# Optimization experiments

Hardware: AMD Instinct MI355X
Metric: run time of the kernel (lower is better)

The kernel has to match this reference:

```python
import jax, jax.numpy as jnp
import numpy as np

H_DIM, N_HEAD, FF_DIM, B_GRAPHS, MAX_N = 256, 8, 1024, 16, 512
LENGTHS = np.array([512, 480, 448, 416, 384, 352, 320, 288] * 2)  # ragged graph sizes, sum = 6400
N_NODES = int(LENGTHS.sum())
N_EDGES = 16 * N_NODES  # avg degree 16


def setup_inputs() -> dict:
    key = jax.random.key(0)
    kq, kk, kv, ko, k1, k2, kh = jax.random.split(key, 7)
    offsets = np.concatenate([[0], np.cumsum(LENGTHS)[:-1]])
    batch_np = np.repeat(np.arange(B_GRAPHS), LENGTHS)
    rng = np.random.default_rng(0)
    src = rng.integers(0, N_NODES, N_EDGES)
    g = batch_np[src]
    dst = offsets[g] + rng.integers(0, LENGTHS[g])  # dst in same graph as src
    edge_index = jnp.asarray(np.stack([src, dst]), dtype=jnp.int32)
    batch = jnp.asarray(batch_np, dtype=jnp.int32)

    def w(k, shape):
        return 0.02 * jax.random.normal(k, shape, dtype=jnp.float32)

    return dict(
        h=jax.random.normal(kh, (N_NODES, H_DIM), dtype=jnp.float32),
        Wq=w(kq, (H_DIM, H_DIM)), bq=jnp.zeros(H_DIM),
        Wk=w(kk, (H_DIM, H_DIM)), bk=jnp.zeros(H_DIM),
        Wv=w(kv, (H_DIM, H_DIM)), bv=jnp.zeros(H_DIM),
        Wo=w(ko, (H_DIM, H_DIM)), bo=jnp.zeros(H_DIM),
        W1=w(k1, (FF_DIM, H_DIM)), b1=jnp.zeros(FF_DIM),
        W2=w(k2, (H_DIM, FF_DIM)), b2=jnp.zeros(H_DIM),
        g1=jnp.ones(H_DIM), be1=jnp.zeros(H_DIM),
        g2=jnp.ones(H_DIM), be2=jnp.zeros(H_DIM),
        batch=batch, edge_index=edge_index,
        num_graphs=B_GRAPHS, max_n=MAX_N, n_head=N_HEAD,
    )


def _layernorm(x, g, b, eps=1e-5):
    mu = x.mean(-1, keepdims=True)
    var = ((x - mu) ** 2).mean(-1, keepdims=True)
    return (x - mu) * jax.lax.rsqrt(var + eps) * g + b


def reference(h, Wq, bq, Wk, bk, Wv, bv, Wo, bo, W1, b1, W2, b2, g1, be1, g2, be2,
              batch, edge_index, num_graphs, max_n, n_head):
    N, H = h.shape
    dh = H // n_head
    # position of each node inside its graph (batch is sorted by graph)
    counts = jax.ops.segment_sum(jnp.ones(N, jnp.int32), batch, num_segments=num_graphs)
    offsets = jnp.concatenate([jnp.zeros(1, jnp.int32), jnp.cumsum(counts)[:-1].astype(jnp.int32)])
    pos = jnp.arange(N, dtype=jnp.int32) - offsets[batch]
    # to_dense_batch: pad ragged nodes into [B, S, H]
    x = jnp.zeros((num_graphs, max_n, H), h.dtype).at[batch, pos].set(h)
    # to_dense_adj + _canonical_mask: faithful to source, EDGES get -inf (True -> -inf)
    src, dst = edge_index[0], edge_index[1]
    adj = jnp.zeros((num_graphs, max_n, max_n), bool).at[batch[src], pos[src], pos[dst]].set(True)
    attn_mask = jnp.where(adj, -jnp.inf, 0.0)[:, None, :, :]  # [B,1,S,S], broadcast over heads

    def proj(W, b):
        return (x @ W.T + b).reshape(num_graphs, max_n, n_head, dh).transpose(0, 2, 1, 3)

    q = proj(Wq, bq)
    k = proj(Wk, bk)
    v = proj(Wk, bk)  # faithful to source: V_x uses self.K
    scores = jax.nn.softmax(attn_mask + jnp.einsum('bhsd,bhtd->bhst', q, k) / np.sqrt(dh).astype(h.dtype), axis=-1)
    att = jnp.einsum('bhst,bhtd->bhsd', scores, v).transpose(0, 2, 1, 3).reshape(num_graphs, max_n, H)
    att = att @ Wo.T + bo
    h_att = att[batch, pos]  # from_dense_batch: unpad back to [N, H]
    h1 = _layernorm(h_att + h, g1, be1)
    ff = jax.nn.relu(h1 @ W1.T + b1) @ W2.T + b2
    return _layernorm(ff + h1, g2, be2)
```

## Files before the change

### kernel.cpp

```cpp
#include <hip/hip_runtime.h>
#include <math.h>

typedef unsigned int u32;
typedef unsigned short ushort_t;
typedef __attribute__((ext_vector_type(8))) short short8;
typedef __attribute__((ext_vector_type(4))) float f32x4;
typedef __attribute__((ext_vector_type(16))) float f32x16;

#define B_G 16
#define S_MAX 512
#define NH 8
#define DH 32
#define HD 256
#define FFD 1024
#define ADJW 16

__device__ __forceinline__ ushort_t f2bf(float f) {
  u32 u = __float_as_uint(f);
  u += 0x7fffu + ((u >> 16) & 1u);
  return (ushort_t)(u >> 16);
}
__device__ __forceinline__ float bf2f(ushort_t s) {
  return __uint_as_float(((u32)s) << 16);
}

__device__ __forceinline__ void gll16(const void* g, void* l) {
  __builtin_amdgcn_global_load_lds(
      (const __attribute__((address_space(1))) unsigned int*)g,
      (__attribute__((address_space(3))) unsigned int*)l, 16, 0, 0);
}

__global__ __launch_bounds__(256) void k_prep2(u32* __restrict__ adj,
    const int* __restrict__ batch, int N, int* __restrict__ offs,
    const float* __restrict__ bq, const float* __restrict__ bk, float* __restrict__ bqk,
    const float* __restrict__ wa, const float* __restrict__ wb, const float* __restrict__ wc,
    const float* __restrict__ wd, const float* __restrict__ we,
    ushort_t* __restrict__ oa, ushort_t* __restrict__ ob, ushort_t* __restrict__ oc,
    ushort_t* __restrict__ od, ushort_t* __restrict__ oe,
    const float* __restrict__ h, ushort_t* __restrict__ hb) {
  int blk = blockIdx.x, tid = threadIdx.x;
  if (blk < 128) {
    uint4 z = {0u, 0u, 0u, 0u};
    ((uint4*)adj)[blk * 256 + tid] = z;
  } else if (blk == 128) {
    bqk[tid] = bq[tid];
    bqk[HD + tid] = bk[tid];
    if (tid <= B_G) {
      if (tid == B_G) { offs[B_G] = N; }
      else {
        int lo = 0, hi = N;
        while (lo < hi) { int mid = (lo + hi) >> 1; if (batch[mid] < tid) lo = mid + 1; else hi = mid; }
        offs[tid] = lo;
      }
    }
  } else if (blk < 481) {
    int bb = blk - 129;
    const float* src; ushort_t* dst; int off;
    if (bb < 32)       { src = wa; dst = oa; off = bb; }
    else if (bb < 64)  { src = wb; dst = ob; off = bb - 32; }
    else if (bb < 96)  { src = wc; dst = oc; off = bb - 64; }
    else if (bb < 224) { src = wd; dst = od; off = bb - 96; }
    else               { src = we; dst = oe; off = bb - 224; }
    size_t i = (size_t)off * 2048 + tid * 8;
    float4 v0 = *(const float4*)&src[i];
    float4 v1 = *(const float4*)&src[i + 4];
    uint4 pk;
    pk.x = (u32)f2bf(v0.x) | ((u32)f2bf(v0.y) << 16);
    pk.y = (u32)f2bf(v0.z) | ((u32)f2bf(v0.w) << 16);
    pk.z = (u32)f2bf(v1.x) | ((u32)f2bf(v1.y) << 16);
    pk.w = (u32)f2bf(v1.z) | ((u32)f2bf(v1.w) << 16);
    *(uint4*)&dst[i] = pk;
  } else {
    size_t i = ((size_t)(blk - 481) * 256 + tid) * 8;
    float4 v0 = *(const float4*)&h[i];
    float4 v1 = *(const float4*)&h[i + 4];
    uint4 pk;
    pk.x = (u32)f2bf(v0.x) | ((u32)f2bf(v0.y) << 16);
    pk.y = (u32)f2bf(v0.z) | ((u32)f2bf(v0.w) << 16);
    pk.z = (u32)f2bf(v1.x) | ((u32)f2bf(v1.y) << 16);
    pk.w = (u32)f2bf(v1.z) | ((u32)f2bf(v1.w) << 16);
    *(uint4*)&hb[i] = pk;
  }
}

__global__ __launch_bounds__(256) void k_qk(const ushort_t* __restrict__ A,
    const ushort_t* __restrict__ W, const float* __restrict__ bias,
    ushort_t* __restrict__ Cout, int gridx,
    const int* __restrict__ ei, int E, const int* __restrict__ batch,
    const int* __restrict__ offs, u32* __restrict__ adj) {
  __shared__ __align__(16) ushort_t As[2][64 * 64];
  __shared__ __align__(16) ushort_t Bs[2][128 * 64];
  int tid = threadIdx.x;
  int wid = tid >> 6, lane = tid & 63;
  int wm = wid & 1, wn = wid >> 1;
  int arow0 = blockIdx.x * 64, bcol0 = blockIdx.y * 128;

  {
    int e = (blockIdx.y * gridx + blockIdx.x) * 256 + tid;
    if (e < E) {
      int s = ei[e], d = ei[E + e];
      int b = batch[s];
      int o = offs[b];
      atomicOr(&adj[(b * S_MAX + (s - o)) * ADJW + ((d - o) >> 5)], 1u << ((d - o) & 31));
    }
  }

  const ushort_t* gA[2]; const ushort_t* gB[4];
  int dofsA[2], dofsB[4];
  #pragma unroll
  for (int i = 0; i < 2; i++) {
    int s = i * 256 + wid * 64 + lane;
    int r = s >> 3, ck = (s & 7) ^ (r & 7);
    gA[i] = A + (size_t)(arow0 + r) * HD + ck * 8;
    dofsA[i] = (i * 256 + wid * 64) * 8;
  }
  #pragma unroll
  for (int i = 0; i < 4; i++) {
    int s = i * 256 + wid * 64 + lane;
    int r = s >> 3, ck = (s & 7) ^ (r & 7);
    gB[i] = W + (size_t)(bcol0 + r) * HD + ck * 8;
    dofsB[i] = (i * 256 + wid * 64) * 8;
  }

  f32x4 acc[2][4];
  #pragma unroll
  for (int i = 0; i < 2; i++)
    #pragma unroll
    for (int j = 0; j < 4; j++) { f32x4 z = {0.f,0.f,0.f,0.f}; acc[i][j] = z; }

  #pragma unroll
  for (int i = 0; i < 2; i++) gll16(gA[i], &As[0][dofsA[i]]);
  #pragma unroll
  for (int i = 0; i < 4; i++) gll16(gB[i], &Bs[0][dofsB[i]]);
  asm volatile("s_waitcnt vmcnt(0)" ::: "memory");
  __builtin_amdgcn_s_barrier();

  int cur = 0;
  for (int ks = 0; ks < 4; ks++) {
    if (ks < 3) {
      int k0n = (ks + 1) << 6;
      #pragma unroll
      for (int i = 0; i < 2; i++) gll16(gA[i] + k0n, &As[cur ^ 1][dofsA[i]]);
      #pragma unroll
      for (int i = 0; i < 4; i++) gll16(gB[i] + k0n, &Bs[cur ^ 1][dofsB[i]]);
      asm volatile("s_waitcnt vmcnt(6)" ::: "memory");
    } else {
      asm volatile("s_waitcnt vmcnt(0)" ::: "memory");
    }
    __builtin_amdgcn_s_barrier();
    #pragma unroll
    for (int kk = 0; kk < 2; kk++) {
      short8 af[2], bfv[4];
      #pragma unroll
      for (int i = 0; i < 2; i++) {
        int row = wm * 32 + i * 16 + (lane & 15);
        int ck = (kk * 4 + (lane >> 4)) ^ (row & 7);
        af[i] = *(const short8*)&As[cur][row * 64 + ck * 8];
      }
      #pragma unroll
      for (int j = 0; j < 4; j++) {
        int row = wn * 64 + j * 16 + (lane & 15);
        int ck = (kk * 4 + (lane >> 4)) ^ (row & 7);
        bfv[j] = *(const short8*)&Bs[cur][row * 64 + ck * 8];
      }
      #pragma unroll
      for (int i = 0; i < 2; i++)
        #pragma unroll
        for (int j = 0; j < 4; j++)
          acc[i][j] = __builtin_amdgcn_mfma_f32_16x16x32_bf16(af[i], bfv[j], acc[i][j], 0, 0, 0);
    }
    __builtin_amdgcn_s_barrier();
    cur ^= 1;
  }

  float bj[4]; int colb[4];
  #pragma unroll
  for (int j = 0; j < 4; j++) {
    colb[j] = bcol0 + wn * 64 + j * 16 + (lane & 15);
    bj[j] = bias[colb[j]];
  }
  #pragma unroll
  for (int i = 0; i < 2; i++) {
    #pragma unroll
    for (int r = 0; r < 4; r++) {
      int row = arow0 + wm * 32 + i * 16 + (lane >> 4) * 4 + r;
      #pragma unroll
      for (int j = 0; j < 4; j++)
        Cout[(size_t)row * 512 + colb[j]] = f2bf(acc[i][j][r] + bj[j]);
    }
  }
}

__global__ __launch_bounds__(256) void k_ffup(const ushort_t* __restrict__ A,
    const ushort_t* __restrict__ W, const float* __restrict__ bias,
    ushort_t* __restrict__ Cout, int Ncols, int Kdim) {
  __shared__ __align__(16) ushort_t As[2][64 * 64];
  __shared__ __align__(16) ushort_t Bs[2][128 * 64];
  int tid = threadIdx.x;
  int wid = tid >> 6, lane = tid & 63;
  int wm = wid & 1, wn = wid >> 1;
  int arow0 = blockIdx.x * 64, bcol0 = blockIdx.y * 128;

  const ushort_t* gA[2]; const ushort_t* gB[4];
  int dofsA[2], dofsB[4];
  #pragma unroll
  for (int i = 0; i < 2; i++) {
    int s = i * 256 + wid * 64 + lane;
    int r = s >> 3, ck = (s & 7) ^ (r & 7);
    gA[i] = A + (size_t)(arow0 + r) * Kdim + ck * 8;
    dofsA[i] = (i * 256 + wid * 64) * 8;
  }
  #pragma unroll
  for (int i = 0; i < 4; i++) {
    int s = i * 256 + wid * 64 + lane;
    int r = s >> 3, ck = (s & 7) ^ (r & 7);
    gB[i] = W + (size_t)(bcol0 + r) * Kdim + ck * 8;
    dofsB[i] = (i * 256 + wid * 64) * 8;
  }

  f32x4 acc[2][4];
  #pragma unroll
  for (int i = 0; i < 2; i++)
    #pragma unroll
    for (int j = 0; j < 4; j++) { f32x4 z = {0.f,0.f,0.f,0.f}; acc[i][j] = z; }

  #pragma unroll
  for (int i = 0; i < 2; i++) gll16(gA[i], &As[0][dofsA[i]]);
  #pragma unroll
  for (int i = 0; i < 4; i++) gll16(gB[i], &Bs[0][dofsB[i]]);
  asm volatile("s_waitcnt vmcnt(0)" ::: "memory");
  __builtin_amdgcn_s_barrier();

  int nsteps = Kdim >> 6;
  int cur = 0;
  for (int ks = 0; ks < nsteps; ks++) {
    if (ks + 1 < nsteps) {
      int k0n = (ks + 1) << 6;
      #pragma unroll
      for (int i = 0; i < 2; i++) gll16(gA[i] + k0n, &As[cur ^ 1][dofsA[i]]);
      #pragma unroll
      for (int i = 0; i < 4; i++) gll16(gB[i] + k0n, &Bs[cur ^ 1][dofsB[i]]);
      asm volatile("s_waitcnt vmcnt(6)" ::: "memory");
    } else {
      asm volatile("s_waitcnt vmcnt(0)" ::: "memory");
    }
    __builtin_amdgcn_s_barrier();
    #pragma unroll
    for (int kk = 0; kk < 2; kk++) {
      short8 af[2], bfv[4];
      #pragma unroll
      for (int i = 0; i < 2; i++) {
        int row = wm * 32 + i * 16 + (lane & 15);
        int ck = (kk * 4 + (lane >> 4)) ^ (row & 7);
        af[i] = *(const short8*)&As[cur][row * 64 + ck * 8];
      }
      #pragma unroll
      for (int j = 0; j < 4; j++) {
        int row = wn * 64 + j * 16 + (lane & 15);
        int ck = (kk * 4 + (lane >> 4)) ^ (row & 7);
        bfv[j] = *(const short8*)&Bs[cur][row * 64 + ck * 8];
      }
      #pragma unroll
      for (int i = 0; i < 2; i++)
        #pragma unroll
        for (int j = 0; j < 4; j++)
          acc[i][j] = __builtin_amdgcn_mfma_f32_16x16x32_bf16(af[i], bfv[j], acc[i][j], 0, 0, 0);
    }
    __builtin_amdgcn_s_barrier();
    cur ^= 1;
  }

  float bj[4]; int colb[4];
  #pragma unroll
  for (int j = 0; j < 4; j++) {
    colb[j] = bcol0 + wn * 64 + j * 16 + (lane & 15);
    bj[j] = bias[colb[j]];
  }
  #pragma unroll
  for (int i = 0; i < 2; i++) {
    #pragma unroll
    for (int r = 0; r < 4; r++) {
      int row = arow0 + wm * 32 + i * 16 + (lane >> 4) * 4 + r;
      #pragma unroll
      for (int j = 0; j < 4; j++)
        Cout[(size_t)row * Ncols + colb[j]] = f2bf(fmaxf(acc[i][j][r] + bj[j], 0.f));
    }
  }
}

template<bool OUTBF>
__global__ __launch_bounds__(256) void k_gemm_ln(const ushort_t* __restrict__ A,
    const ushort_t* __restrict__ W, const float* __restrict__ bias,
    const float* __restrict__ R, const float* __restrict__ gamma,
    const float* __restrict__ beta, float* __restrict__ outF,
    ushort_t* __restrict__ outB, int Kdim) {
  __shared__ __align__(16) ushort_t As[2][32 * 64];
  __shared__ __align__(16) ushort_t Bs[2][256 * 64];
  __shared__ float red_s[32 * 4];
  __shared__ float red_q[32 * 4];
  int tid = threadIdx.x;
  int wid = tid >> 6, lane = tid & 63;
  int wn = wid;
  int row0 = blockIdx.x * 32;

  const ushort_t* gA; int dofsA;
  {
    int r = tid >> 3, ck = (tid & 7) ^ (r & 7);
    gA = A + (size_t)(row0 + r) * Kdim + ck * 8;
    dofsA = (wid * 64) * 8;
  }
  const ushort_t* gB[8]; int dofsB[8];
  #pragma unroll
  for (int i = 0; i < 8; i++) {
    int s = i * 256 + tid;
    int r = s >> 3, ck = (s & 7) ^ (r & 7);
    gB[i] = W + (size_t)r * Kdim + ck * 8;
    dofsB[i] = (i * 256 + wid * 64) * 8;
  }

  f32x4 acc[2][4];
  #pragma unroll
  for (int i = 0; i < 2; i++)
    #pragma unroll
    for (int n = 0; n < 4; n++) { f32x4 z = {0.f,0.f,0.f,0.f}; acc[i][n] = z; }

  gll16(gA, &As[0][dofsA]);
  #pragma unroll
  for (int i = 0; i < 8; i++) gll16(gB[i], &Bs[0][dofsB[i]]);
  asm volatile("s_waitcnt vmcnt(0)" ::: "memory");
  __builtin_amdgcn_s_barrier();

  int nsteps = Kdim >> 6;
  int cur = 0;
  for (int ks = 0; ks < nsteps; ks++) {
    if (ks + 1 < nsteps) {
      int k0n = (ks + 1) << 6;
      gll16(gA + k0n, &As[cur ^ 1][dofsA]);
      #pragma unroll
      for (int i = 0; i < 8; i++) gll16(gB[i] + k0n, &Bs[cur ^ 1][dofsB[i]]);
      asm volatile("s_waitcnt vmcnt(9)" ::: "memory");
    } else {
      asm volatile("s_waitcnt vmcnt(0)" ::: "memory");
    }
    __builtin_amdgcn_s_barrier();
    #pragma unroll
    for (int kk = 0; kk < 2; kk++) {
      short8 af[2], bfv[4];
      #pragma unroll
      for (int i = 0; i < 2; i++) {
        int row = i * 16 + (lane & 15);
        int ck = (kk * 4 + (lane >> 4)) ^ (row & 7);
        af[i] = *(const short8*)&As[cur][row * 64 + ck * 8];
      }
      #pragma unroll
      for (int n = 0; n < 4; n++) {
        int row = wn * 64 + n * 16 + (lane & 15);
        int ck = (kk * 4 + (lane >> 4)) ^ (row & 7);
        bfv[n] = *(const short8*)&Bs[cur][row * 64 + ck * 8];
      }
      #pragma unroll
      for (int i = 0; i < 2; i++)
        #pragma unroll
        for (int n = 0; n < 4; n++)
          acc[i][n] = __builtin_amdgcn_mfma_f32_16x16x32_bf16(af[i], bfv[n], acc[i][n], 0, 0, 0);
    }
    __builtin_amdgcn_s_barrier();
    cur ^= 1;
  }

  int col[4]; float bc[4], gm[4], bt[4];
  #pragma unroll
  for (int n = 0; n < 4; n++) {
    col[n] = wn * 64 + n * 16 + (lane & 15);
    bc[n] = bias[col[n]]; gm[n] = gamma[col[n]]; bt[n] = beta[col[n]];
  }
  #pragma unroll
  for (int i = 0; i < 2; i++) {
    #pragma unroll
    for (int r = 0; r < 4; r++) {
      int row_l = i * 16 + (lane >> 4) * 4 + r;
      const float* Rrow = R + (size_t)(row0 + row_l) * HD;
      float s = 0.f, q = 0.f;
      #pragma unroll
      for (int n = 0; n < 4; n++) {
        float v = acc[i][n][r] + bc[n] + Rrow[col[n]];
        acc[i][n][r] = v;
        s += v; q += v * v;
      }
      #pragma unroll
      for (int o = 1; o < 16; o <<= 1) { s += __shfl_xor(s, o, 64); q += __shfl_xor(q, o, 64); }
      if ((lane & 15) == 0) { red_s[row_l * 4 + wn] = s; red_q[row_l * 4 + wn] = q; }
    }
  }
  __syncthreads();
  #pragma unroll
  for (int i = 0; i < 2; i++) {
    #pragma unroll
    for (int r = 0; r < 4; r++) {
      int row_l = i * 16 + (lane >> 4) * 4 + r;
      float ssum = red_s[row_l * 4] + red_s[row_l * 4 + 1] + red_s[row_l * 4 + 2] + red_s[row_l * 4 + 3];
      float qsum = red_q[row_l * 4] + red_q[row_l * 4 + 1] + red_q[row_l * 4 + 2] + red_q[row_l * 4 + 3];
      float mu = ssum * (1.f / HD);
      float var = qsum * (1.f / HD) - mu * mu;
      float inv = rsqrtf(var + 1e-5f);
      size_t rb = (size_t)(row0 + row_l) * HD;
      #pragma unroll
      for (int n = 0; n < 4; n++) {
        float v = (acc[i][n][r] - mu) * inv * gm[n] + bt[n];
        outF[rb + col[n]] = v;
        if (OUTBF) outB[rb + col[n]] = f2bf(v);
      }
    }
  }
}

__global__ __launch_bounds__(256) void k_attn(const ushort_t* __restrict__ qkb,
    const u32* __restrict__ adj, const int* __restrict__ offs,
    const float* __restrict__ bqk, ushort_t* __restrict__ attOb) {
  int bid = blockIdx.x;
  int qtr = bid & 3, hh = (bid >> 2) & 7, b = bid >> 5;
  int nstart = offs[b], len = offs[b + 1] - nstart;
  int q0blk = qtr * 128;
  if (q0blk >= len) return;
  int lenT = len >> 5;

  __shared__ __align__(16) ushort_t K_lds[4 * 512 * 8];
  __shared__ __align__(16) ushort_t Kt_lds[64 * 32 * 8];
  __shared__ __align__(16) ushort_t P_lds[4 * 4 * 32 * 8];

  int tid = threadIdx.x;
  {
    const ushort_t* kg = qkb + (size_t)nstart * 512 + 256 + hh * 32;
    for (int t = tid; t < len; t += 256) {
      const uint4* src = (const uint4*)(kg + (size_t)t * 512);
      uint4 v0 = src[0], v1 = src[1], v2 = src[2], v3 = src[3];
      *(uint4*)&K_lds[0 * 4096 + t * 8] = v0;
      *(uint4*)&K_lds[1 * 4096 + t * 8] = v1;
      *(uint4*)&K_lds[2 * 4096 + t * 8] = v2;
      *(uint4*)&K_lds[3 * 4096 + t * 8] = v3;
    }
  }
  __syncthreads();
  {
    int d = tid & 31, tg = tid >> 5;
    int cc = d >> 3, e = d & 7;
    for (int i = 0; i < 8; i++) {
      int t0 = tg * 64 + i * 8;
      if (t0 < len) {
        u32 w0 = (u32)K_lds[cc * 4096 + (t0 + 0) * 8 + e] | ((u32)K_lds[cc * 4096 + (t0 + 1) * 8 + e] << 16);
        u32 w1 = (u32)K_lds[cc * 4096 + (t0 + 2) * 8 + e] | ((u32)K_lds[cc * 4096 + (t0 + 3) * 8 + e] << 16);
        u32 w2 = (u32)K_lds[cc * 4096 + (t0 + 4) * 8 + e] | ((u32)K_lds[cc * 4096 + (t0 + 5) * 8 + e] << 16);
        u32 w3 = (u32)K_lds[cc * 4096 + (t0 + 6) * 8 + e] | ((u32)K_lds[cc * 4096 + (t0 + 7) * 8 + e] << 16);
        uint4 pk = {w0, w1, w2, w3};
        *(uint4*)&Kt_lds[(t0 >> 3) * 256 + d * 8] = pk;
      }
    }
  }
  __syncthreads();

  int w = tid >> 6, lane = tid & 63;
  int q0w = q0blk + w * 32;
  if (q0w >= len) return;

  int lq = lane & 31, hf = lane >> 5;
  const float SCALE = 0.17677669529663687f;

  size_t qrow = (size_t)(nstart + q0w + lq) * 512 + hh * 32;
  short8 qf0 = *(const short8*)(qkb + qrow + hf * 8);
  short8 qf1 = *(const short8*)(qkb + qrow + 16 + hf * 8);

  const uint4* ap = (const uint4*)(adj + (size_t)(b * S_MAX + q0w + lq) * ADJW);
  uint4 a0 = ap[0], a1 = ap[1], a2 = ap[2], a3 = ap[3];
  u32 aw[16] = {a0.x, a0.y, a0.z, a0.w, a1.x, a1.y, a1.z, a1.w,
                a2.x, a2.y, a2.z, a2.w, a3.x, a3.y, a3.z, a3.w};

  f32x16 oacc = {0.f,0.f,0.f,0.f,0.f,0.f,0.f,0.f,0.f,0.f,0.f,0.f,0.f,0.f,0.f,0.f};
  float lsum = 0.f;

  for (int tt = 0; tt < lenT; tt++) {
    int t0 = tt * 32;
    short8 ka0 = *(const short8*)&K_lds[hf * 4096 + (t0 + lq) * 8];
    short8 ka1 = *(const short8*)&K_lds[(2 + hf) * 4096 + (t0 + lq) * 8];
    f32x16 sc = {0.f,0.f,0.f,0.f,0.f,0.f,0.f,0.f,0.f,0.f,0.f,0.f,0.f,0.f,0.f,0.f};
    sc = __builtin_amdgcn_mfma_f32_32x32x16_bf16(ka0, qf0, sc, 0, 0, 0);
    sc = __builtin_amdgcn_mfma_f32_32x32x16_bf16(ka1, qf1, sc, 0, 0, 0);
    u32 word = aw[tt];
    float p[16];
    #pragma unroll
    for (int r = 0; r < 16; r++) {
      int tb = (r & 3) + 8 * (r >> 2) + 4 * hf;
      float pe = __expf(sc[r] * SCALE);
      p[r] = ((word >> tb) & 1u) ? 0.f : pe;
      lsum += p[r];
    }
    #pragma unroll
    for (int g = 0; g < 4; g++) {
      u32 lo = (u32)f2bf(p[4 * g]) | ((u32)f2bf(p[4 * g + 1]) << 16);
      u32 hi = (u32)f2bf(p[4 * g + 2]) | ((u32)f2bf(p[4 * g + 3]) << 16);
      uint2 pk = {lo, hi};
      *(uint2*)&P_lds[w * 1024 + g * 256 + lq * 8 + hf * 4] = pk;
    }
    short8 va0 = *(const short8*)&Kt_lds[(t0 / 8 + hf) * 256 + lq * 8];
    short8 va1 = *(const short8*)&Kt_lds[(t0 / 8 + 2 + hf) * 256 + lq * 8];
    short8 pb0 = *(const short8*)&P_lds[w * 1024 + hf * 256 + lq * 8];
    short8 pb1 = *(const short8*)&P_lds[w * 1024 + (2 + hf) * 256 + lq * 8];
    oacc = __builtin_amdgcn_mfma_f32_32x32x16_bf16(va0, pb0, oacc, 0, 0, 0);
    oacc = __builtin_amdgcn_mfma_f32_32x32x16_bf16(va1, pb1, oacc, 0, 0, 0);
  }

  const float* bkh = bqk + 256 + hh * 32;
  float pq = 0.f;
  #pragma unroll
  for (int j = 0; j < 8; j++) pq += bf2f((ushort_t)qf0[j]) * bkh[hf * 8 + j];
  #pragma unroll
  for (int j = 0; j < 8; j++) pq += bf2f((ushort_t)qf1[j]) * bkh[16 + hf * 8 + j];
  pq += __shfl_xor(pq, 32, 64);
  float pe_pad = __expf(pq * SCALE) * (float)(S_MAX - len);

  float ltot = lsum + __shfl_xor(lsum, 32, 64) + pe_pad;
  float inv = 1.f / ltot;
  {
    int node = nstart + q0w + lq;
    ushort_t* op = attOb + (size_t)node * HD + hh * DH;
    #pragma unroll
    for (int g = 0; g < 4; g++) {
      float v0 = (oacc[4 * g]     + pe_pad * bkh[g * 8 + hf * 4 + 0]) * inv;
      float v1 = (oacc[4 * g + 1] + pe_pad * bkh[g * 8 + hf * 4 + 1]) * inv;
      float v2 = (oacc[4 * g + 2] + pe_pad * bkh[g * 8 + hf * 4 + 2]) * inv;
      float v3 = (oacc[4 * g + 3] + pe_pad * bkh[g * 8 + hf * 4 + 3]) * inv;
      u32 lo = (u32)f2bf(v0) | ((u32)f2bf(v1) << 16);
      u32 hi = (u32)f2bf(v2) | ((u32)f2bf(v3) << 16);
      uint2 pk = {lo, hi};
      *(uint2*)(op + g * 8 + hf * 4) = pk;
    }
  }
}

extern "C" void kernel_launch(void* const* d_in, const int* in_sizes, int n_in,
                              void* d_out, int out_size, void* d_ws, size_t ws_size,
                              hipStream_t stream) {
  const float* h   = (const float*)d_in[0];
  const float* Wq  = (const float*)d_in[1];
  const float* bq  = (const float*)d_in[2];
  const float* Wk  = (const float*)d_in[3];
  const float* bk  = (const float*)d_in[4];
  const float* Wo  = (const float*)d_in[7];
  const float* bo  = (const float*)d_in[8];
  const float* W1  = (const float*)d_in[9];
  const float* b1  = (const float*)d_in[10];
  const float* W2  = (const float*)d_in[11];
  const float* b2  = (const float*)d_in[12];
  const float* g1  = (const float*)d_in[13];
  const float* be1 = (const float*)d_in[14];
  const float* g2  = (const float*)d_in[15];
  const float* be2 = (const float*)d_in[16];
  const int* batch = (const int*)d_in[17];
  const int* ei    = (const int*)d_in[18];
  int N = in_sizes[0] / HD;
  int E = in_sizes[18] / 2;

  char* ws = (char*)d_ws;
  ushort_t* hb    = (ushort_t*)(ws);
  ushort_t* attOb = hb;
  ushort_t* qkb   = (ushort_t*)(ws + ((size_t)4 << 20));
  float*    h1    = (float*)(ws + ((size_t)12 << 20));
  ushort_t* h1b   = (ushort_t*)(ws + ((size_t)19 << 20));
  ushort_t* ff1b  = (ushort_t*)(ws + ((size_t)23 << 20));
  char* wbase = ws + ((size_t)36 << 20);
  ushort_t* Wqkb = (ushort_t*)(wbase);
  ushort_t* Wob  = (ushort_t*)(wbase + (256 << 10));
  ushort_t* W1b  = (ushort_t*)(wbase + (384 << 10));
  ushort_t* W2b  = (ushort_t*)(wbase + (896 << 10));
  float*    bqk  = (float*)(wbase + (1408 << 10));
  u32*      adj  = (u32*)(wbase + (1536 << 10));
  int*      offs = (int*)(ws + ((size_t)38 << 20));

  k_prep2<<<1281, 256, 0, stream>>>(adj, batch, N, offs, bq, bk, bqk,
                                    Wq, Wk, Wo, W1, W2,
                                    Wqkb, Wqkb + 65536, Wob, W1b, W2b, h, hb);
  k_qk<<<dim3(100, 4), 256, 0, stream>>>(hb, Wqkb, bqk, qkb, 100,
                                         ei, E, batch, offs, adj);
  k_attn<<<B_G * NH * 4, 256, 0, stream>>>(qkb, adj, offs, bqk, attOb);
  k_gemm_ln<true><<<200, 256, 0, stream>>>(attOb, Wob, bo, h, g1, be1, h1, h1b, HD);
  k_ffup<<<dim3(100, 8), 256, 0, stream>>>(h1b, W1b, b1, ff1b, FFD, HD);
  k_gemm_ln<false><<<200, 256, 0, stream>>>(ff1b, W2b, b2, h1, g2, be2, (float*)d_out, nullptr, FFD);
}
```

Before: 86.66 us.

## Keep P in registers via permlane swap, enlarge attention blocks, use bf16 residual

The attention kernel now builds the bf16 P operand for the PV MFMA with v_permlane32_swap instead of writing it to LDS and reading it back, which removes the P_lds round trip. It also launches 512-thread blocks covering half a graph each, so each K/Kt tile loaded into LDS serves twice as many query rows. The first LayerNorm GEMM no longer writes the fp32 h1, and the second one reads the bf16 h1 as its residual, cutting global traffic at some cost in residual precision.

Result: no change. 85.09 us (-1.8%).

```diff
diff --git a/kernel.cpp b/kernel.cpp
--- a/kernel.cpp
+++ b/kernel.cpp
@@ -6,6 +6,7 @@
 typedef __attribute__((ext_vector_type(8))) short short8;
 typedef __attribute__((ext_vector_type(4))) float f32x4;
 typedef __attribute__((ext_vector_type(16))) float f32x16;
+typedef __attribute__((ext_vector_type(4))) unsigned int u32x4;
 
 #define B_G 16
 #define S_MAX 512
@@ -288,10 +289,10 @@
   }
 }
 
-template<bool OUTBF>
+template<bool OUTF, bool OUTBF, bool RESBF>
 __global__ __launch_bounds__(256) void k_gemm_ln(const ushort_t* __restrict__ A,
     const ushort_t* __restrict__ W, const float* __restrict__ bias,
-    const float* __restrict__ R, const float* __restrict__ gamma,
+    const void* __restrict__ R, const float* __restrict__ gamma,
     const float* __restrict__ beta, float* __restrict__ outF,
     ushort_t* __restrict__ outB, int Kdim) {
   __shared__ __align__(16) ushort_t As[2][32 * 64];
@@ -379,11 +380,13 @@
     #pragma unroll
     for (int r = 0; r < 4; r++) {
       int row_l = i * 16 + (lane >> 4) * 4 + r;
-      const float* Rrow = R + (size_t)(row0 + row_l) * HD;
+      size_t rbase = (size_t)(row0 + row_l) * HD;
       float s = 0.f, q = 0.f;
       #pragma unroll
       for (int n = 0; n < 4; n++) {
-        float v = acc[i][n][r] + bc[n] + Rrow[col[n]];
+        float rv = RESBF ? bf2f(((const ushort_t*)R)[rbase + col[n]])
+                         : ((const float*)R)[rbase + col[n]];
+        float v = acc[i][n][r] + bc[n] + rv;
         acc[i][n][r] = v;
         s += v; q += v * v;
       }
@@ -407,31 +410,28 @@
       #pragma unroll
       for (int n = 0; n < 4; n++) {
         float v = (acc[i][n][r] - mu) * inv * gm[n] + bt[n];
-        outF[rb + col[n]] = v;
+        if (OUTF) outF[rb + col[n]] = v;
         if (OUTBF) outB[rb + col[n]] = f2bf(v);
       }
     }
   }
 }
 
-__global__ __launch_bounds__(256) void k_attn(const ushort_t* __restrict__ qkb,
+__global__ __launch_bounds__(512) void k_attn(const ushort_t* __restrict__ qkb,
     const u32* __restrict__ adj, const int* __restrict__ offs,
     const float* __restrict__ bqk, ushort_t* __restrict__ attOb) {
   int bid = blockIdx.x;
-  int qtr = bid & 3, hh = (bid >> 2) & 7, b = bid >> 5;
+  int half = bid & 1, hh = (bid >> 1) & 7, b = bid >> 4;
   int nstart = offs[b], len = offs[b + 1] - nstart;
-  int q0blk = qtr * 128;
-  if (q0blk >= len) return;
   int lenT = len >> 5;
 
   __shared__ __align__(16) ushort_t K_lds[4 * 512 * 8];
   __shared__ __align__(16) ushort_t Kt_lds[64 * 32 * 8];
-  __shared__ __align__(16) ushort_t P_lds[4 * 4 * 32 * 8];
 
   int tid = threadIdx.x;
   {
     const ushort_t* kg = qkb + (size_t)nstart * 512 + 256 + hh * 32;
-    for (int t = tid; t < len; t += 256) {
+    for (int t = tid; t < len; t += 512) {
       const uint4* src = (const uint4*)(kg + (size_t)t * 512);
       uint4 v0 = src[0], v1 = src[1], v2 = src[2], v3 = src[3];
       *(uint4*)&K_lds[0 * 4096 + t * 8] = v0;
@@ -444,8 +444,9 @@
   {
     int d = tid & 31, tg = tid >> 5;
     int cc = d >> 3, e = d & 7;
-    for (int i = 0; i < 8; i++) {
-      int t0 = tg * 64 + i * 8;
+    #pragma unroll
+    for (int i = 0; i < 4; i++) {
+      int t0 = tg * 32 + i * 8;
       if (t0 < len) {
         u32 w0 = (u32)K_lds[cc * 4096 + (t0 + 0) * 8 + e] | ((u32)K_lds[cc * 4096 + (t0 + 1) * 8 + e] << 16);
         u32 w1 = (u32)K_lds[cc * 4096 + (t0 + 2) * 8 + e] | ((u32)K_lds[cc * 4096 + (t0 + 3) * 8 + e] << 16);
@@ -459,7 +460,7 @@
   __syncthreads();
 
   int w = tid >> 6, lane = tid & 63;
-  int q0w = q0blk + w * 32;
+  int q0w = half * 256 + w * 32;
   if (q0w >= len) return;
 
   int lq = lane & 31, hf = lane >> 5;
@@ -493,17 +494,24 @@
       p[r] = ((word >> tb) & 1u) ? 0.f : pe;
       lsum += p[r];
     }
-    #pragma unroll
-    for (int g = 0; g < 4; g++) {
-      u32 lo = (u32)f2bf(p[4 * g]) | ((u32)f2bf(p[4 * g + 1]) << 16);
-      u32 hi = (u32)f2bf(p[4 * g + 2]) | ((u32)f2bf(p[4 * g + 3]) << 16);
-      uint2 pk = {lo, hi};
-      *(uint2*)&P_lds[w * 1024 + g * 256 + lq * 8 + hf * 4] = pk;
-    }
+    u32 q0 = (u32)f2bf(p[0])  | ((u32)f2bf(p[1])  << 16);
+    u32 q1 = (u32)f2bf(p[2])  | ((u32)f2bf(p[3])  << 16);
+    u32 q2 = (u32)f2bf(p[4])  | ((u32)f2bf(p[5])  << 16);
+    u32 q3 = (u32)f2bf(p[6])  | ((u32)f2bf(p[7])  << 16);
+    u32 q4 = (u32)f2bf(p[8])  | ((u32)f2bf(p[9])  << 16);
+    u32 q5 = (u32)f2bf(p[10]) | ((u32)f2bf(p[11]) << 16);
+    u32 q6 = (u32)f2bf(p[12]) | ((u32)f2bf(p[13]) << 16);
+    u32 q7 = (u32)f2bf(p[14]) | ((u32)f2bf(p[15]) << 16);
+    asm volatile("v_permlane32_swap_b32 %0, %1" : "+v"(q0), "+v"(q2));
+    asm volatile("v_permlane32_swap_b32 %0, %1" : "+v"(q1), "+v"(q3));
+    asm volatile("v_permlane32_swap_b32 %0, %1" : "+v"(q4), "+v"(q6));
+    asm volatile("v_permlane32_swap_b32 %0, %1" : "+v"(q5), "+v"(q7));
+    u32x4 f0v = {q0, q1, q2, q3};
+    u32x4 f1v = {q4, q5, q6, q7};
+    short8 pb0 = __builtin_bit_cast(short8, f0v);
+    short8 pb1 = __builtin_bit_cast(short8, f1v);
     short8 va0 = *(const short8*)&Kt_lds[(t0 / 8 + hf) * 256 + lq * 8];
     short8 va1 = *(const short8*)&Kt_lds[(t0 / 8 + 2 + hf) * 256 + lq * 8];
-    short8 pb0 = *(const short8*)&P_lds[w * 1024 + hf * 256 + lq * 8];
-    short8 pb1 = *(const short8*)&P_lds[w * 1024 + (2 + hf) * 256 + lq * 8];
     oacc = __builtin_amdgcn_mfma_f32_32x32x16_bf16(va0, pb0, oacc, 0, 0, 0);
     oacc = __builtin_amdgcn_mfma_f32_32x32x16_bf16(va1, pb1, oacc, 0, 0, 0);
   }
@@ -563,7 +571,6 @@
   ushort_t* hb    = (ushort_t*)(ws);
   ushort_t* attOb = hb;
   ushort_t* qkb   = (ushort_t*)(ws + ((size_t)4 << 20));
-  float*    h1    = (float*)(ws + ((size_t)12 << 20));
   ushort_t* h1b   = (ushort_t*)(ws + ((size_t)19 << 20));
   ushort_t* ff1b  = (ushort_t*)(ws + ((size_t)23 << 20));
   char* wbase = ws + ((size_t)36 << 20);
@@ -580,8 +587,10 @@
                                     Wqkb, Wqkb + 65536, Wob, W1b, W2b, h, hb);
   k_qk<<<dim3(100, 4), 256, 0, stream>>>(hb, Wqkb, bqk, qkb, 100,
                                          ei, E, batch, offs, adj);
-  k_attn<<<B_G * NH * 4, 256, 0, stream>>>(qkb, adj, offs, bqk, attOb);
-  k_gemm_ln<true><<<200, 256, 0, stream>>>(attOb, Wob, bo, h, g1, be1, h1, h1b, HD);
+  k_attn<<<B_G * NH * 2, 512, 0, stream>>>(qkb, adj, offs, bqk, attOb);
+  k_gemm_ln<false, true, false><<<200, 256, 0, stream>>>(attOb, Wob, bo, h, g1, be1,
+                                                         nullptr, h1b, HD);
   k_ffup<<<dim3(100, 8), 256, 0, stream>>>(h1b, W1b, b1, ff1b, FFD, HD);
-  k_gemm_ln<false><<<200, 256, 0, stream>>>(ff1b, W2b, b2, h1, g2, be2, (float*)d_out, nullptr, FFD);
-}
+  k_gemm_ln<true, false, true><<<200, 256, 0, stream>>>(ff1b, W2b, b2, h1b, g2, be2,
+                                                        (float*)d_out, nullptr, FFD);
+}
```
